# Optimization experiments

Hardware: AMD Instinct MI355X
Metric: run time of the kernel (lower is better)

The kernel has to match this reference:

```python
import jax, jax.numpy as jnp
import numpy as np

N, E, H, NH = 10000, 160000, 128, 8
HD = H // NH
LDIM = 8  # (lmax+1)**2 - 1 with lmax=2
CUTOFF = 5.0


def setup_inputs() -> dict:
    key = jax.random.key(0)
    ks = jax.random.split(key, 20)
    w = lambda k, shape: jax.random.normal(k, shape, jnp.float32) * 0.05
    return dict(
        node_feats=jax.random.normal(ks[0], (N, H), jnp.float32),
        edge_feats=jax.random.normal(ks[1], (E, H), jnp.float32),
        vector_feats=jax.random.normal(ks[2], (N, LDIM, H), jnp.float32),
        distances=jax.random.uniform(ks[3], (E,), jnp.float32) * CUTOFF,
        d_ij=jax.random.normal(ks[4], (E, LDIM), jnp.float32),
        senders=jax.random.randint(ks[5], (E,), 0, N),
        receivers=jax.random.randint(ks[6], (E,), 0, N),
        ln_scale=jnp.ones((H,), jnp.float32),
        ln_bias=jnp.zeros((H,), jnp.float32),
        vln_w=jnp.ones((H,), jnp.float32),
        W_vec=w(ks[7], (H, 3 * H)),
        Wq=w(ks[8], (H, H)), bq=jnp.zeros((H,), jnp.float32),
        Wk=w(ks[9], (H, H)), bk=jnp.zeros((H,), jnp.float32),
        Wv=w(ks[10], (H, H)), bv=jnp.zeros((H,), jnp.float32),
        Wdk=w(ks[11], (H, H)), bdk=jnp.zeros((H,), jnp.float32),
        Wdv=w(ks[12], (H, H)), bdv=jnp.zeros((H,), jnp.float32),
        Ws=w(ks[13], (H, 2 * H)), bs=jnp.zeros((2 * H,), jnp.float32),
        Wo=w(ks[14], (H, 3 * H)), bo=jnp.zeros((3 * H,), jnp.float32),
        Wf=w(ks[15], (H, H)), bf=jnp.zeros((H,), jnp.float32),
        Wsrc=w(ks[16], (H, H)),
        Wtrg=w(ks[17], (H, H)),
    )


def _reject(vec, d):
    # vector rejection of vec [E, L, H] against direction d [E, L]
    proj = (vec * d[:, :, None]).sum(axis=1, keepdims=True)
    return vec - proj * d[:, :, None]


def _forward(node_feats, edge_feats, vector_feats, distances, d_ij, senders, receivers,
             ln_scale, ln_bias, vln_w, W_vec, Wq, bq, Wk, bk, Wv, bv, Wdk, bdk, Wdv, bdv,
             Ws, bs, Wo, bo, Wf, bf, Wsrc, Wtrg):
    silu = jax.nn.silu
    n = node_feats.shape[0]
    # LayerNorm (eps=1e-5) on node feats
    mu = node_feats.mean(-1, keepdims=True)
    xc = node_feats - mu
    var = (xc * xc).mean(-1, keepdims=True)
    x = xc * jax.lax.rsqrt(var + 1e-5) * ln_scale + ln_bias
    # VecLayerNorm with norm_type='none' -> identity norm + learned per-channel scale
    vec = vector_feats * vln_w
    q = (x @ Wq + bq).reshape(-1, NH, HD)
    k = (x @ Wk + bk).reshape(-1, NH, HD)
    v = (x @ Wv + bv).reshape(-1, NH, HD)
    dk = silu(edge_feats @ Wdk + bdk).reshape(-1, NH, HD)
    dv = silu(edge_feats @ Wdv + bdv).reshape(-1, NH, HD)
    vec1, vec2, vec3 = jnp.split(vec @ W_vec, [H, 2 * H], axis=-1)
    vec_dot = (vec1 * vec2).sum(axis=1)  # [N, H]
    # per-edge gathers
    q_i = q[receivers]
    k_j = k[senders]
    v_j = v[senders]
    vec_j = vec[senders]  # [E, LDIM, H]
    # attention-style message with cosine cutoff
    cut = 0.5 * (jnp.cos(distances * (jnp.pi / CUTOFF)) + 1.0) * (distances < CUTOFF)
    attn = silu((q_i * k_j * dk).sum(-1)) * cut[:, None]  # [E, NH]
    vj = ((v_j * dv) * attn[:, :, None]).reshape(-1, H)   # [E, H]
    s1, s2 = jnp.split(silu(vj @ Ws + bs), [H], axis=1)
    vec_msg = vec_j * s1[:, None, :] + s2[:, None, :] * d_ij[:, :, None]
    # scatter reduce to nodes
    node_agg = jax.ops.segment_sum(vj, receivers, num_segments=n)
    vec_agg = jax.ops.segment_sum(vec_msg, receivers, num_segments=n)
    o1, o2, o3 = jnp.split(node_agg @ Wo + bo, [H, 2 * H], axis=1)
    dx = vec_dot * o2 + o3
    dvec = vec3 * o1[:, None, :] + vec_agg
    # edge update (last_layer=False)
    w1 = _reject(vec[receivers] @ Wtrg, d_ij)
    w2 = _reject(vec_j @ Wsrc, -d_ij)
    w_dot = (w1 * w2).sum(axis=1)  # [E, H]
    df_ij = silu(edge_feats @ Wf + bf) * w_dot
    return dx, df_ij, dvec


def reference(node_feats, edge_feats, vector_feats, distances, d_ij, senders, receivers,
              ln_scale, ln_bias, vln_w, W_vec, Wq, bq, Wk, bk, Wv, bv, Wdk, bdk, Wdv, bdv,
              Ws, bs, Wo, bo, Wf, bf, Wsrc, Wtrg):
    return _forward(node_feats, edge_feats, vector_feats, distances, d_ij, senders, receivers,
                    ln_scale, ln_bias, vln_w, W_vec, Wq, bq, Wk, bk, Wv, bv, Wdk, bdk, Wdv, bdv,
                    Ws, bs, Wo, bo, Wf, bf, Wsrc, Wtrg)
```

## Files before the change

### kernel.cpp

```cpp
#include <hip/hip_runtime.h>
#include <math.h>

#define NN 10000
#define NE 160000
#define H  128
#define LD 8

typedef unsigned short ushort_t;
typedef short bf16x8 __attribute__((ext_vector_type(8)));
typedef float f32x4 __attribute__((ext_vector_type(4)));

__device__ __forceinline__ float silu_f(float x){ return x / (1.0f + expf(-x)); }
__device__ __forceinline__ float4 f4z(){ return make_float4(0.f,0.f,0.f,0.f); }

__device__ __forceinline__ void fma4(float4& acc, float s, const float4 w){
    acc.x = fmaf(s, w.x, acc.x);
    acc.y = fmaf(s, w.y, acc.y);
    acc.z = fmaf(s, w.z, acc.z);
    acc.w = fmaf(s, w.w, acc.w);
}

__device__ __forceinline__ float4 silu4(float4 a, float4 b){
    return make_float4(silu_f(a.x+b.x), silu_f(a.y+b.y), silu_f(a.z+b.z), silu_f(a.w+b.w));
}

__device__ __forceinline__ ushort_t f2bf(float f){
    union { float f; unsigned int u; } x; x.f = f;
    unsigned int r = x.u + 0x7FFFu + ((x.u >> 16) & 1u);
    return (ushort_t)(r >> 16);
}
__device__ __forceinline__ unsigned int pack2bf(float a, float b){
    return (unsigned int)f2bf(a) | ((unsigned int)f2bf(b) << 16);
}
__device__ __forceinline__ float bf2f_hi(unsigned int u){
    union { unsigned int u; float f; } x; x.u = u & 0xffff0000u; return x.f;
}
__device__ __forceinline__ float bf2f_lo(unsigned int u){
    union { unsigned int u; float f; } x; x.u = u << 16; return x.f;
}

__global__ void k_prepw(const float* __restrict__ Wq, const float* __restrict__ Wk,
                        const float* __restrict__ Wv, const float* __restrict__ W_vec,
                        const float* __restrict__ Wtrg, const float* __restrict__ Wsrc,
                        const float* __restrict__ Wdk, const float* __restrict__ Wdv,
                        const float* __restrict__ Ws,
                        ushort_t* __restrict__ wqkvT, ushort_t* __restrict__ wvecT,
                        ushort_t* __restrict__ wdkT, ushort_t* __restrict__ wdvT,
                        ushort_t* __restrict__ wsT){
    int i = blockIdx.x * 256 + threadIdx.x;
    int n = i >> 7, kk = i & 127;
    if (n < 384){
        float v;
        if (n < 128)      v = Wq[kk*128 + n];
        else if (n < 256) v = Wk[kk*128 + (n-128)];
        else              v = Wv[kk*128 + (n-256)];
        wqkvT[n*128 + kk] = f2bf(v);
    } else if (n < 1024){
        int m = n - 384;
        float v;
        if (m < 384)      v = W_vec[kk*384 + m];
        else if (m < 512) v = Wtrg[kk*128 + (m-384)];
        else              v = Wsrc[kk*128 + (m-512)];
        wvecT[m*128 + kk] = f2bf(v);
    } else if (n < 1152){
        int m = n - 1024;
        wdkT[m*128 + kk] = f2bf(Wdk[kk*128 + m]);
    } else if (n < 1280){
        int m = n - 1152;
        wdvT[m*128 + kk] = f2bf(Wdv[kk*128 + m]);
    } else if (n < 1536){
        int m = n - 1280;
        wsT[m*128 + kk] = f2bf(Ws[kk*256 + m]);
    }
}

__global__ void k_ef2bf(const float* __restrict__ ef, ushort_t* __restrict__ ef_bf){
    size_t i = (size_t)blockIdx.x * 256 + threadIdx.x;
    const float4* s = (const float4*)ef;
    float4 a = s[2*i], b = s[2*i+1];
    uint4 u;
    u.x = pack2bf(a.x, a.y); u.y = pack2bf(a.z, a.w);
    u.z = pack2bf(b.x, b.y); u.w = pack2bf(b.z, b.w);
    ((uint4*)ef_bf)[i] = u;
}

__global__ void k_hist(const int* __restrict__ rcv, int* __restrict__ cnt){
    int e = blockIdx.x * 256 + threadIdx.x;
    if (e < NE) atomicAdd(&cnt[rcv[e]], 1);
}

__global__ __launch_bounds__(256) void k_scan(const int* __restrict__ cnt, int* __restrict__ offs){
    __shared__ int part[256];
    const int t = threadIdx.x;
    const int CH = 40;
    int loc[CH];
    int base = t * CH;
    int lsum = 0;
    if (base < NN){
        #pragma unroll
        for (int i = 0; i < CH; i++){ loc[i] = cnt[base + i]; lsum += loc[i]; }
    }
    part[t] = lsum;
    __syncthreads();
    for (int off = 1; off < 256; off <<= 1){
        int v = (t >= off) ? part[t - off] : 0;
        __syncthreads();
        part[t] += v;
        __syncthreads();
    }
    int ex = part[t] - lsum;
    if (base < NN){
        int run = ex;
        #pragma unroll
        for (int i = 0; i < CH; i++){ offs[base + i] = run; run += loc[i]; }
    }
    if (t == 255) offs[NN] = part[255];
}

__global__ void k_scatter(const int* __restrict__ rcv, const int* __restrict__ offs,
                          int* __restrict__ cnt2, int* __restrict__ eidx){
    int e = blockIdx.x * 256 + threadIdx.x;
    if (e < NE){
        int r = rcv[e];
        int p = atomicAdd(&cnt2[r], 1);
        eidx[offs[r] + p] = e;
    }
}

__global__ __launch_bounds__(128) void node_ln(
    const float* __restrict__ nf, const float* __restrict__ vf,
    const float* __restrict__ ln_s, const float* __restrict__ ln_b,
    const float* __restrict__ vlnw,
    ushort_t* __restrict__ x_bf, ushort_t* __restrict__ vec_bf)
{
    const int n = blockIdx.x, h = threadIdx.x;
    __shared__ float red[4];
    float xv = nf[(size_t)n*H + h];
    float s1 = xv, s2 = xv*xv;
    #pragma unroll
    for (int o = 32; o >= 1; o >>= 1){
        s1 += __shfl_xor(s1, o, 64);
        s2 += __shfl_xor(s2, o, 64);
    }
    const int wid = h >> 6;
    if ((h & 63) == 0){ red[wid] = s1; red[2+wid] = s2; }
    __syncthreads();
    float mean = (red[0] + red[1]) * (1.0f/H);
    float var  = (red[2] + red[3]) * (1.0f/H) - mean*mean;
    float x = (xv - mean) * rsqrtf(var + 1e-5f) * ln_s[h] + ln_b[h];
    x_bf[(size_t)n*H + h] = f2bf(x);
    float w = vlnw[h];
    #pragma unroll
    for (int l = 0; l < LD; l++){
        size_t i = ((size_t)n*LD + l)*H + h;
        vec_bf[i] = f2bf(vf[i] * w);
    }
}

__global__ __launch_bounds__(256) void node_qkv(
    const ushort_t* __restrict__ x_bf, const ushort_t* __restrict__ wqkvT,
    const float* __restrict__ bq, const float* __restrict__ bk, const float* __restrict__ bv,
    float* __restrict__ q, float* __restrict__ k, float* __restrict__ v)
{
    const int tid  = threadIdx.x;
    const int lane = tid & 63;
    const int m0   = (tid >> 6) * 16;
    const int e0   = blockIdx.x * 64;

    const int mrow = lane & 15;
    const int kblk = lane >> 4;

    f32x4 acc[24];
    #pragma unroll
    for (int nt = 0; nt < 24; nt++) acc[nt] = (f32x4)(0.f);

    int arow = e0 + m0 + mrow; if (arow >= NN) arow = NN-1;
    const ushort_t* Arow = x_bf + (size_t)arow*H + kblk*8;
    const ushort_t* wb   = wqkvT + (size_t)mrow*H + kblk*8;

    #pragma unroll
    for (int ks = 0; ks < 4; ks++){
        bf16x8 a = *(const bf16x8*)(Arow + ks*32);
        #pragma unroll
        for (int nt = 0; nt < 24; nt++){
            bf16x8 b8 = *(const bf16x8*)(wb + (size_t)nt*16*H + ks*32);
            acc[nt] = __builtin_amdgcn_mfma_f32_16x16x32_bf16(a, b8, acc[nt], 0, 0, 0);
        }
    }
    float* outs[3] = {q, k, v};
    const float* bias[3] = {bq, bk, bv};
    #pragma unroll
    for (int g = 0; g < 3; g++){
        #pragma unroll
        for (int t = 0; t < 8; t++){
            int col = t*16 + mrow;
            float bb = bias[g][col];
            #pragma unroll
            for (int r = 0; r < 4; r++){
                int row = e0 + m0 + kblk*4 + r;
                if (row < NN) outs[g][(size_t)row*H + col] = acc[g*8+t][r] + bb;
            }
        }
    }
}

__global__ __launch_bounds__(256) void node_vec(
    const ushort_t* __restrict__ vec_bf, const ushort_t* __restrict__ wvecT,
    float* __restrict__ vdot, ushort_t* __restrict__ vec3,
    ushort_t* __restrict__ Vt, ushort_t* __restrict__ Vs)
{
    __shared__ ushort_t st_s[64][136];

    const int tid  = threadIdx.x;
    const int lane = tid & 63;
    const int wv   = tid >> 6;
    const int m0   = wv * 16;
    const size_t r0 = (size_t)blockIdx.x * 64;

    const int mrow = lane & 15;
    const int kblk = lane >> 4;

    f32x4 acc[40];
    #pragma unroll
    for (int nt = 0; nt < 40; nt++) acc[nt] = (f32x4)(0.f);

    const ushort_t* Arow = vec_bf + (r0 + m0 + mrow)*H + kblk*8;
    const ushort_t* wb   = wvecT + (size_t)mrow*H + kblk*8;

    #pragma unroll
    for (int ks = 0; ks < 4; ks++){
        bf16x8 a = *(const bf16x8*)(Arow + ks*32);
        #pragma unroll
        for (int nt = 0; nt < 40; nt++){
            bf16x8 b8 = *(const bf16x8*)(wb + (size_t)nt*16*H + ks*32);
            acc[nt] = __builtin_amdgcn_mfma_f32_16x16x32_bf16(a, b8, acc[nt], 0, 0, 0);
        }
    }

    #pragma unroll
    for (int t = 0; t < 8; t++){
        float p = acc[t][0]*acc[t+8][0] + acc[t][1]*acc[t+8][1]
                + acc[t][2]*acc[t+8][2] + acc[t][3]*acc[t+8][3];
        p += __shfl_xor(p, 16, 64);
        if ((kblk & 1) == 0){
            int node = (int)(r0 >> 3) + wv*2 + (kblk >> 1);
            vdot[(size_t)node*H + t*16 + mrow] = p;
        }
    }

    ushort_t* outs[3] = {vec3, Vt, Vs};
    #pragma unroll
    for (int g = 0; g < 3; g++){
        __syncthreads();
        #pragma unroll
        for (int t = 0; t < 8; t++){
            int coln = t*16 + mrow;
            int lr = m0 + kblk*4;
            st_s[lr+0][coln] = f2bf(acc[16+g*8+t][0]);
            st_s[lr+1][coln] = f2bf(acc[16+g*8+t][1]);
            st_s[lr+2][coln] = f2bf(acc[16+g*8+t][2]);
            st_s[lr+3][coln] = f2bf(acc[16+g*8+t][3]);
        }
        __syncthreads();
        const int rr = tid >> 2, qq = tid & 3;
        uint4* dst = (uint4*)&outs[g][(r0 + rr)*H + qq*32];
        const uint4* src = (const uint4*)&st_s[rr][qq*32];
        dst[0] = src[0]; dst[1] = src[1]; dst[2] = src[2]; dst[3] = src[3];
    }
}

__global__ __launch_bounds__(256) void edge_attn(
    const ushort_t* __restrict__ ef_bf,
    const ushort_t* __restrict__ wdkT, const float* __restrict__ bdk,
    const ushort_t* __restrict__ wdvT, const float* __restrict__ bdv,
    const int* __restrict__ snd, const int* __restrict__ rcv,
    const float* __restrict__ dist,
    const float* __restrict__ q, const float* __restrict__ k, const float* __restrict__ v,
    ushort_t* __restrict__ vj)
{
    __shared__ ushort_t dk_s[64][136];
    __shared__ ushort_t dv_s[64][136];

    const int tid  = threadIdx.x;
    const int lane = tid & 63;
    const int m0   = (tid >> 6) * 16;
    const size_t e0 = (size_t)blockIdx.x * 64;

    const int mrow = lane & 15;
    const int kblk = lane >> 4;

    f32x4 accK[8], accV[8];
    #pragma unroll
    for (int nt = 0; nt < 8; nt++){ accK[nt] = (f32x4)(0.f); accV[nt] = (f32x4)(0.f); }

    const ushort_t* Arow = ef_bf + (e0 + m0 + mrow)*H + kblk*8;
    const ushort_t* wkb  = wdkT + (size_t)mrow*H + kblk*8;
    const ushort_t* wvb  = wdvT + (size_t)mrow*H + kblk*8;

    #pragma unroll
    for (int ks = 0; ks < 4; ks++){
        bf16x8 a = *(const bf16x8*)(Arow + ks*32);
        #pragma unroll
        for (int nt = 0; nt < 8; nt++){
            bf16x8 bk8 = *(const bf16x8*)(wkb + (size_t)nt*16*H + ks*32);
            accK[nt] = __builtin_amdgcn_mfma_f32_16x16x32_bf16(a, bk8, accK[nt], 0, 0, 0);
            bf16x8 bv8 = *(const bf16x8*)(wvb + (size_t)nt*16*H + ks*32);
            accV[nt] = __builtin_amdgcn_mfma_f32_16x16x32_bf16(a, bv8, accV[nt], 0, 0, 0);
        }
    }

    const int lrow = m0 + 4*kblk;
    #pragma unroll
    for (int nt = 0; nt < 8; nt++){
        int coln = nt*16 + mrow;
        float bkn = bdk[coln], bvn = bdv[coln];
        #pragma unroll
        for (int r = 0; r < 4; r++){
            dk_s[lrow + r][coln] = f2bf(silu_f(accK[nt][r] + bkn));
            dv_s[lrow + r][coln] = f2bf(silu_f(accV[nt][r] + bvn));
        }
    }
    __syncthreads();

    const int r  = tid >> 2, cq = tid & 3;
    const size_t e = e0 + r;
    const int s  = snd[e], rr = rcv[e];
    const float d = dist[e];
    const float cut = (d < 5.0f) ? 0.5f*(cosf(d*0.6283185307179586f) + 1.0f) : 0.0f;
    const float* qrow = q + (size_t)rr*H + cq*32;
    const float* krow = k + (size_t)s*H + cq*32;
    const float* vrow = v + (size_t)s*H + cq*32;
    ushort_t* vjrow = vj + e*H + cq*32;

    #pragma unroll
    for (int hh = 0; hh < 2; hh++){
        const int c0 = hh*16;
        float p = 0.f;
        #pragma unroll
        for (int j = 0; j < 4; j++){
            float4 q4 = *(const float4*)(qrow + c0 + 4*j);
            float4 k4 = *(const float4*)(krow + c0 + 4*j);
            uint2 du = *(const uint2*)&dk_s[r][cq*32 + c0 + 4*j];
            p += q4.x*k4.x*bf2f_lo(du.x) + q4.y*k4.y*bf2f_hi(du.x)
               + q4.z*k4.z*bf2f_lo(du.y) + q4.w*k4.w*bf2f_hi(du.y);
        }
        float attn = silu_f(p) * cut;
        #pragma unroll
        for (int j = 0; j < 4; j++){
            float4 v4 = *(const float4*)(vrow + c0 + 4*j);
            uint2 du = *(const uint2*)&dv_s[r][cq*32 + c0 + 4*j];
            uint2 u;
            u.x = pack2bf(v4.x*bf2f_lo(du.x)*attn, v4.y*bf2f_hi(du.x)*attn);
            u.y = pack2bf(v4.z*bf2f_lo(du.y)*attn, v4.w*bf2f_hi(du.y)*attn);
            *(uint2*)(vjrow + c0 + 4*j) = u;
        }
    }
}

__global__ __launch_bounds__(256) void edge_s(
    const ushort_t* __restrict__ vj, const ushort_t* __restrict__ wsT,
    const float* __restrict__ bs, ushort_t* __restrict__ s12)
{
    __shared__ ushort_t s_s[64][264];

    const int tid  = threadIdx.x;
    const int lane = tid & 63;
    const int m0   = (tid >> 6) * 16;
    const size_t e0 = (size_t)blockIdx.x * 64;

    const int mrow = lane & 15;
    const int kblk = lane >> 4;

    f32x4 acc[16];
    #pragma unroll
    for (int nt = 0; nt < 16; nt++) acc[nt] = (f32x4)(0.f);

    const ushort_t* Arow = vj + (e0 + m0 + mrow)*H + kblk*8;
    const ushort_t* wb   = wsT + (size_t)mrow*H + kblk*8;

    #pragma unroll
    for (int ks = 0; ks < 4; ks++){
        bf16x8 a = *(const bf16x8*)(Arow + ks*32);
        #pragma unroll
        for (int nt = 0; nt < 16; nt++){
            bf16x8 b8 = *(const bf16x8*)(wb + (size_t)nt*16*H + ks*32);
            acc[nt] = __builtin_amdgcn_mfma_f32_16x16x32_bf16(a, b8, acc[nt], 0, 0, 0);
        }
    }

    const int lrow = m0 + 4*kblk;
    #pragma unroll
    for (int nt = 0; nt < 16; nt++){
        int coln = nt*16 + mrow;
        float bb = bs[coln];
        #pragma unroll
        for (int r = 0; r < 4; r++)
            s_s[lrow + r][coln] = f2bf(silu_f(acc[nt][r] + bb));
    }
    __syncthreads();

    const int r = tid >> 2, cq = tid & 3;
    const uint4* srcp = (const uint4*)&s_s[r][cq*64];
    uint4* dstp = (uint4*)&s12[(e0 + r)*256 + cq*64];
    #pragma unroll
    for (int j = 0; j < 8; j++) dstp[j] = srcp[j];
}

__global__ __launch_bounds__(256) void edge_df(
    const float* __restrict__ ef, const float* __restrict__ Wf, const float* __restrict__ bf_,
    const int* __restrict__ eidx,
    const int* __restrict__ snd, const int* __restrict__ rcv,
    const float* __restrict__ dij,
    const ushort_t* __restrict__ Vt, const ushort_t* __restrict__ Vs,
    float* __restrict__ df)
{
    __shared__ float wf_s[H][32];
    __shared__ float e_s[32][H+4];
    __shared__ int   eidx_s[32];
    __shared__ int   snd_s[32];
    __shared__ int   rcv_s[32];
    __shared__ float dij_s[32][LD];

    const int tid = threadIdx.x;
    const int by  = blockIdx.y;
    const int p0  = blockIdx.x * 32;

    if (tid < 32) eidx_s[tid] = eidx[p0 + tid];
    __syncthreads();
    if (tid < 32){ int e = eidx_s[tid]; snd_s[tid] = snd[e]; rcv_s[tid] = rcv[e]; }
    for (int i = tid; i < 32*LD; i += 256){
        int row = i >> 3, l = i & 7;
        dij_s[row][l] = dij[(size_t)eidx_s[row]*LD + l];
    }
    for (int i = tid; i < H*8; i += 256){
        int row = i >> 3, c4 = i & 7;
        *(float4*)&wf_s[row][c4*4] = *(const float4*)&Wf[row*H + by*32 + c4*4];
    }
    for (int i = tid; i < 32*32; i += 256){
        int row = i >> 5, c4 = i & 31;
        *(float4*)&e_s[row][c4*4] = *(const float4*)&ef[(size_t)eidx_s[row]*H + c4*4];
    }
    __syncthreads();

    const int g = tid & 7, r0 = tid >> 3;
    float4 af = f4z();
    for (int kk = 0; kk < H; kk++){
        float4 w4 = *(float4*)&wf_s[kk][g*4];
        fma4(af, e_s[r0][kk], w4);
    }
    float4 bf4 = *(const float4*)&bf_[by*32 + g*4];
    float4 f4v = silu4(af, bf4);

    const int e = eidx_s[r0];
    const int s = snd_s[r0], rr = rcv_s[r0];
    const ushort_t* Ar = Vt + (size_t)rr*LD*H + by*32 + g*4;
    const ushort_t* Br = Vs + (size_t)s*LD*H + by*32 + g*4;

    float4 AB = f4z(), aa = f4z(), bb = f4z();
    float dd = 0.f;
    #pragma unroll
    for (int l = 0; l < LD; l++){
        float dl = dij_s[r0][l];
        dd = fmaf(dl, dl, dd);
        uint2 ua = *(const uint2*)&Ar[(size_t)l*H];
        uint2 ub = *(const uint2*)&Br[(size_t)l*H];
        float Ax = bf2f_lo(ua.x), Ay = bf2f_hi(ua.x), Az = bf2f_lo(ua.y), Aw = bf2f_hi(ua.y);
        float Bx = bf2f_lo(ub.x), By = bf2f_hi(ub.x), Bz = bf2f_lo(ub.y), Bw = bf2f_hi(ub.y);
        AB.x = fmaf(Ax, Bx, AB.x); AB.y = fmaf(Ay, By, AB.y);
        AB.z = fmaf(Az, Bz, AB.z); AB.w = fmaf(Aw, Bw, AB.w);
        aa.x = fmaf(Ax, dl, aa.x); aa.y = fmaf(Ay, dl, aa.y);
        aa.z = fmaf(Az, dl, aa.z); aa.w = fmaf(Aw, dl, aa.w);
        bb.x = fmaf(Bx, dl, bb.x); bb.y = fmaf(By, dl, bb.y);
        bb.z = fmaf(Bz, dl, bb.z); bb.w = fmaf(Bw, dl, bb.w);
    }
    float c = 2.0f - dd;
    float4 o = make_float4(f4v.x*(AB.x - aa.x*bb.x*c),
                           f4v.y*(AB.y - aa.y*bb.y*c),
                           f4v.z*(AB.z - aa.z*bb.z*c),
                           f4v.w*(AB.w - aa.w*bb.w*c));
    *(float4*)&df[(size_t)e*H + by*32 + g*4] = o;
}

__global__ __launch_bounds__(256) void node_gather(
    const int* __restrict__ offs, const int* __restrict__ eidx, const int* __restrict__ snd,
    const ushort_t* __restrict__ vj, const ushort_t* __restrict__ s12,
    const float* __restrict__ dij, const ushort_t* __restrict__ vec,
    const float* __restrict__ Wo, const float* __restrict__ bo,
    const float* __restrict__ vdot, const ushort_t* __restrict__ vec3,
    float* __restrict__ dx, float* __restrict__ dvec)
{
    const int n = blockIdx.x;
    const int tid = threadIdx.x;
    const int h = tid & 127;
    const int par = tid >> 7;
    const int beg = offs[n], end = offs[n+1];
    float na = 0.f;
    float av[LD];
    #pragma unroll
    for (int l = 0; l < LD; l++) av[l] = 0.f;

    for (int i = beg + par; i < end; i += 2){
        int e = eidx[i];
        int s = snd[e];
        float vjv = bf2f_lo((unsigned int)vj[(size_t)e*H + h]);
        float s1 = bf2f_lo((unsigned int)s12[(size_t)e*256 + h]);
        float s2 = bf2f_lo((unsigned int)s12[(size_t)e*256 + 128 + h]);
        na += vjv;
        float4 d0 = *(const float4*)&dij[(size_t)e*LD];
        float4 d1 = *(const float4*)&dij[(size_t)e*LD + 4];
        const ushort_t* vr = &vec[(size_t)s*LD*H + h];
        av[0] = fmaf(bf2f_lo((unsigned int)vr[0*H]), s1, fmaf(d0.x, s2, av[0]));
        av[1] = fmaf(bf2f_lo((unsigned int)vr[1*H]), s1, fmaf(d0.y, s2, av[1]));
        av[2] = fmaf(bf2f_lo((unsigned int)vr[2*H]), s1, fmaf(d0.z, s2, av[2]));
        av[3] = fmaf(bf2f_lo((unsigned int)vr[3*H]), s1, fmaf(d0.w, s2, av[3]));
        av[4] = fmaf(bf2f_lo((unsigned int)vr[4*H]), s1, fmaf(d1.x, s2, av[4]));
        av[5] = fmaf(bf2f_lo((unsigned int)vr[5*H]), s1, fmaf(d1.y, s2, av[5]));
        av[6] = fmaf(bf2f_lo((unsigned int)vr[6*H]), s1, fmaf(d1.z, s2, av[6]));
        av[7] = fmaf(bf2f_lo((unsigned int)vr[7*H]), s1, fmaf(d1.w, s2, av[7]));
    }

    __shared__ float red_s[LD+1][128];
    if (par == 0){
        #pragma unroll
        for (int l = 0; l < LD; l++) red_s[l][h] = av[l];
        red_s[LD][h] = na;
    }
    __syncthreads();
    if (par == 1){
        #pragma unroll
        for (int l = 0; l < LD; l++) red_s[l][h] += av[l];
        red_s[LD][h] += na;
    }
    __syncthreads();

    if (par == 0){
        float o1 = bo[h], o2 = bo[H + h], o3 = bo[2*H + h];
        for (int kk = 0; kk < H; kk++){
            float a = red_s[LD][kk];
            o1 = fmaf(a, Wo[kk*(3*H) + h], o1);
            o2 = fmaf(a, Wo[kk*(3*H) + H + h], o2);
            o3 = fmaf(a, Wo[kk*(3*H) + 2*H + h], o3);
        }
        dx[(size_t)n*H + h] = fmaf(vdot[(size_t)n*H + h], o2, o3);
        #pragma unroll
        for (int l = 0; l < LD; l++){
            size_t i2 = ((size_t)n*LD + l)*H + h;
            dvec[i2] = fmaf(bf2f_lo((unsigned int)vec3[i2]), o1, red_s[l][h]);
        }
    }
}

extern "C" void kernel_launch(void* const* d_in, const int* in_sizes, int n_in,
                              void* d_out, int out_size, void* d_ws, size_t ws_size,
                              hipStream_t stream) {
    const float* nf    = (const float*)d_in[0];
    const float* ef    = (const float*)d_in[1];
    const float* vf    = (const float*)d_in[2];
    const float* dist  = (const float*)d_in[3];
    const float* dij   = (const float*)d_in[4];
    const int*   snd   = (const int*)d_in[5];
    const int*   rcv   = (const int*)d_in[6];
    const float* ln_s  = (const float*)d_in[7];
    const float* ln_b  = (const float*)d_in[8];
    const float* vlnw  = (const float*)d_in[9];
    const float* W_vec = (const float*)d_in[10];
    const float* Wq    = (const float*)d_in[11];
    const float* bq    = (const float*)d_in[12];
    const float* Wk    = (const float*)d_in[13];
    const float* bk    = (const float*)d_in[14];
    const float* Wv    = (const float*)d_in[15];
    const float* bv    = (const float*)d_in[16];
    const float* Wdk   = (const float*)d_in[17];
    const float* bdk   = (const float*)d_in[18];
    const float* Wdv   = (const float*)d_in[19];
    const float* bdv   = (const float*)d_in[20];
    const float* Ws    = (const float*)d_in[21];
    const float* bs    = (const float*)d_in[22];
    const float* Wo    = (const float*)d_in[23];
    const float* bo    = (const float*)d_in[24];
    const float* Wf    = (const float*)d_in[25];
    const float* bf_   = (const float*)d_in[26];
    const float* Wsrc  = (const float*)d_in[27];
    const float* Wtrg  = (const float*)d_in[28];

    float* out  = (float*)d_out;
    float* dx   = out;
    float* df   = out + (size_t)NN*H;
    float* dvec = df + (size_t)NE*H;

    float* w = (float*)d_ws;
    size_t off = 0;
    float* q    = w + off; off += (size_t)NN*H;
    float* k    = w + off; off += (size_t)NN*H;
    float* v    = w + off; off += (size_t)NN*H;
    float* vdot = w + off; off += (size_t)NN*H;
    ushort_t* x_bf   = (ushort_t*)(w + off); off += (size_t)NN*H/2;
    ushort_t* vec_bf = (ushort_t*)(w + off); off += (size_t)NN*LD*H/2;
    ushort_t* vec3   = (ushort_t*)(w + off); off += (size_t)NN*LD*H/2;
    ushort_t* Vt     = (ushort_t*)(w + off); off += (size_t)NN*LD*H/2;
    ushort_t* Vs     = (ushort_t*)(w + off); off += (size_t)NN*LD*H/2;
    ushort_t* vj     = (ushort_t*)(w + off); off += (size_t)NE*H/2;
    ushort_t* s12    = (ushort_t*)(w + off); off += (size_t)NE*256/2;
    ushort_t* ef_bf  = s12;
    ushort_t* wqkvT = (ushort_t*)(w + off); off += 384*128/2;
    ushort_t* wvecT = (ushort_t*)(w + off); off += 640*128/2;
    ushort_t* wdkT  = (ushort_t*)(w + off); off += 128*128/2;
    ushort_t* wdvT  = (ushort_t*)(w + off); off += 128*128/2;
    ushort_t* wsT   = (ushort_t*)(w + off); off += 256*128/2;
    int* cnt  = (int*)(w + off); off += NN;
    int* cnt2 = (int*)(w + off); off += NN;
    int* offs = (int*)(w + off); off += NN + 1;
    int* eidx = (int*)(w + off); off += NE;

    hipMemsetAsync(cnt,  0, NN*sizeof(int), stream);
    hipMemsetAsync(cnt2, 0, NN*sizeof(int), stream);

    k_prepw<<<768, 256, 0, stream>>>(Wq, Wk, Wv, W_vec, Wtrg, Wsrc, Wdk, Wdv, Ws,
                                     wqkvT, wvecT, wdkT, wdvT, wsT);
    k_ef2bf<<<NE*H/8/256, 256, 0, stream>>>(ef, ef_bf);

    k_hist<<<(NE+255)/256, 256, 0, stream>>>(rcv, cnt);
    k_scan<<<1, 256, 0, stream>>>(cnt, offs);
    k_scatter<<<(NE+255)/256, 256, 0, stream>>>(rcv, offs, cnt2, eidx);

    node_ln<<<NN, 128, 0, stream>>>(nf, vf, ln_s, ln_b, vlnw, x_bf, vec_bf);

    node_qkv<<<(NN+63)/64, 256, 0, stream>>>(x_bf, wqkvT, bq, bk, bv, q, k, v);

    node_vec<<<NN*LD/64, 256, 0, stream>>>(vec_bf, wvecT, vdot, vec3, Vt, Vs);

    edge_attn<<<NE/64, 256, 0, stream>>>(ef_bf, wdkT, bdk, wdvT, bdv, snd, rcv, dist,
                                         q, k, v, vj);

    edge_df<<<dim3(NE/32, 4), 256, 0, stream>>>(ef, Wf, bf_, eidx, snd, rcv, dij, Vt, Vs, df);

    edge_s<<<NE/64, 256, 0, stream>>>(vj, wsT, bs, s12);

    node_gather<<<NN, 256, 0, stream>>>(offs, eidx, snd, vj, s12, dij, vec_bf,
                                        Wo, bo, vdot, vec3, dx, dvec);
}
```

Measured before the change: 831.7 us.

## Store k/v in bf16, widen edge_df column tile, and split node_gather four ways

Three separate changes. The k and v projections are stored as bf16 so the per-edge sender gathers in edge_attn read half the bytes. edge_df now handles 64 columns per block with two row passes, halving how often edge_feats is reloaded and the matmul redone across the y grid. node_gather runs 512 threads, splits edges four ways, and spreads the Wo projection over three thread groups. Together these add bf16 rounding on k and v, more shared memory, and an extra barrier in node_gather.

```diff
diff --git a/kernel.cpp b/kernel.cpp
--- a/kernel.cpp
+++ b/kernel.cpp
@@ -160,7 +160,7 @@
 __global__ __launch_bounds__(256) void node_qkv(
     const ushort_t* __restrict__ x_bf, const ushort_t* __restrict__ wqkvT,
     const float* __restrict__ bq, const float* __restrict__ bk, const float* __restrict__ bv,
-    float* __restrict__ q, float* __restrict__ k, float* __restrict__ v)
+    float* __restrict__ q, ushort_t* __restrict__ k_bf, ushort_t* __restrict__ v_bf)
 {
     const int tid  = threadIdx.x;
     const int lane = tid & 63;
@@ -187,19 +187,34 @@
             acc[nt] = __builtin_amdgcn_mfma_f32_16x16x32_bf16(a, b8, acc[nt], 0, 0, 0);
         }
     }
-    float* outs[3] = {q, k, v};
-    const float* bias[3] = {bq, bk, bv};
-    #pragma unroll
-    for (int g = 0; g < 3; g++){
-        #pragma unroll
-        for (int t = 0; t < 8; t++){
-            int col = t*16 + mrow;
-            float bb = bias[g][col];
-            #pragma unroll
-            for (int r = 0; r < 4; r++){
-                int row = e0 + m0 + kblk*4 + r;
-                if (row < NN) outs[g][(size_t)row*H + col] = acc[g*8+t][r] + bb;
-            }
+    #pragma unroll
+    for (int t = 0; t < 8; t++){
+        int col = t*16 + mrow;
+        float bb = bq[col];
+        #pragma unroll
+        for (int r = 0; r < 4; r++){
+            int row = e0 + m0 + kblk*4 + r;
+            if (row < NN) q[(size_t)row*H + col] = acc[t][r] + bb;
+        }
+    }
+    #pragma unroll
+    for (int t = 0; t < 8; t++){
+        int col = t*16 + mrow;
+        float bb = bk[col];
+        #pragma unroll
+        for (int r = 0; r < 4; r++){
+            int row = e0 + m0 + kblk*4 + r;
+            if (row < NN) k_bf[(size_t)row*H + col] = f2bf(acc[8+t][r] + bb);
+        }
+    }
+    #pragma unroll
+    for (int t = 0; t < 8; t++){
+        int col = t*16 + mrow;
+        float bb = bv[col];
+        #pragma unroll
+        for (int r = 0; r < 4; r++){
+            int row = e0 + m0 + kblk*4 + r;
+            if (row < NN) v_bf[(size_t)row*H + col] = f2bf(acc[16+t][r] + bb);
         }
     }
 }
@@ -275,7 +290,8 @@
     const ushort_t* __restrict__ wdvT, const float* __restrict__ bdv,
     const int* __restrict__ snd, const int* __restrict__ rcv,
     const float* __restrict__ dist,
-    const float* __restrict__ q, const float* __restrict__ k, const float* __restrict__ v,
+    const float* __restrict__ q, const ushort_t* __restrict__ k_bf,
+    const ushort_t* __restrict__ v_bf,
     ushort_t* __restrict__ vj)
 {
     __shared__ ushort_t dk_s[64][136];
@@ -327,9 +343,9 @@
     const int s  = snd[e], rr = rcv[e];
     const float d = dist[e];
     const float cut = (d < 5.0f) ? 0.5f*(cosf(d*0.6283185307179586f) + 1.0f) : 0.0f;
-    const float* qrow = q + (size_t)rr*H + cq*32;
-    const float* krow = k + (size_t)s*H + cq*32;
-    const float* vrow = v + (size_t)s*H + cq*32;
+    const float*    qrow = q    + (size_t)rr*H + cq*32;
+    const ushort_t* krow = k_bf + (size_t)s*H + cq*32;
+    const ushort_t* vrow = v_bf + (size_t)s*H + cq*32;
     ushort_t* vjrow = vj + e*H + cq*32;
 
     #pragma unroll
@@ -339,19 +355,21 @@
         #pragma unroll
         for (int j = 0; j < 4; j++){
             float4 q4 = *(const float4*)(qrow + c0 + 4*j);
-            float4 k4 = *(const float4*)(krow + c0 + 4*j);
+            uint2 ku = *(const uint2*)(krow + c0 + 4*j);
             uint2 du = *(const uint2*)&dk_s[r][cq*32 + c0 + 4*j];
-            p += q4.x*k4.x*bf2f_lo(du.x) + q4.y*k4.y*bf2f_hi(du.x)
-               + q4.z*k4.z*bf2f_lo(du.y) + q4.w*k4.w*bf2f_hi(du.y);
+            p += q4.x*bf2f_lo(ku.x)*bf2f_lo(du.x) + q4.y*bf2f_hi(ku.x)*bf2f_hi(du.x)
+               + q4.z*bf2f_lo(ku.y)*bf2f_lo(du.y) + q4.w*bf2f_hi(ku.y)*bf2f_hi(du.y);
         }
         float attn = silu_f(p) * cut;
         #pragma unroll
         for (int j = 0; j < 4; j++){
-            float4 v4 = *(const float4*)(vrow + c0 + 4*j);
+            uint2 vu = *(const uint2*)(vrow + c0 + 4*j);
             uint2 du = *(const uint2*)&dv_s[r][cq*32 + c0 + 4*j];
             uint2 u;
-            u.x = pack2bf(v4.x*bf2f_lo(du.x)*attn, v4.y*bf2f_hi(du.x)*attn);
-            u.y = pack2bf(v4.z*bf2f_lo(du.y)*attn, v4.w*bf2f_hi(du.y)*attn);
+            u.x = pack2bf(bf2f_lo(vu.x)*bf2f_lo(du.x)*attn,
+                          bf2f_hi(vu.x)*bf2f_hi(du.x)*attn);
+            u.y = pack2bf(bf2f_lo(vu.y)*bf2f_lo(du.y)*attn,
+                          bf2f_hi(vu.y)*bf2f_hi(du.y)*attn);
             *(uint2*)(vjrow + c0 + 4*j) = u;
         }
     }
@@ -414,7 +432,7 @@
     const ushort_t* __restrict__ Vt, const ushort_t* __restrict__ Vs,
     float* __restrict__ df)
 {
-    __shared__ float wf_s[H][32];
+    __shared__ float wf_s[H][64];
     __shared__ float e_s[32][H+4];
     __shared__ int   eidx_s[32];
     __shared__ int   snd_s[32];
@@ -432,9 +450,9 @@
         int row = i >> 3, l = i & 7;
         dij_s[row][l] = dij[(size_t)eidx_s[row]*LD + l];
     }
-    for (int i = tid; i < H*8; i += 256){
-        int row = i >> 3, c4 = i & 7;
-        *(float4*)&wf_s[row][c4*4] = *(const float4*)&Wf[row*H + by*32 + c4*4];
+    for (int i = tid; i < H*16; i += 256){
+        int row = i >> 4, c4 = i & 15;
+        *(float4*)&wf_s[row][c4*4] = *(const float4*)&Wf[row*H + by*64 + c4*4];
     }
     for (int i = tid; i < 32*32; i += 256){
         int row = i >> 5, c4 = i & 31;
@@ -442,46 +460,50 @@
     }
     __syncthreads();
 
-    const int g = tid & 7, r0 = tid >> 3;
-    float4 af = f4z();
-    for (int kk = 0; kk < H; kk++){
-        float4 w4 = *(float4*)&wf_s[kk][g*4];
-        fma4(af, e_s[r0][kk], w4);
-    }
-    float4 bf4 = *(const float4*)&bf_[by*32 + g*4];
-    float4 f4v = silu4(af, bf4);
-
-    const int e = eidx_s[r0];
-    const int s = snd_s[r0], rr = rcv_s[r0];
-    const ushort_t* Ar = Vt + (size_t)rr*LD*H + by*32 + g*4;
-    const ushort_t* Br = Vs + (size_t)s*LD*H + by*32 + g*4;
-
-    float4 AB = f4z(), aa = f4z(), bb = f4z();
-    float dd = 0.f;
-    #pragma unroll
-    for (int l = 0; l < LD; l++){
-        float dl = dij_s[r0][l];
-        dd = fmaf(dl, dl, dd);
-        uint2 ua = *(const uint2*)&Ar[(size_t)l*H];
-        uint2 ub = *(const uint2*)&Br[(size_t)l*H];
-        float Ax = bf2f_lo(ua.x), Ay = bf2f_hi(ua.x), Az = bf2f_lo(ua.y), Aw = bf2f_hi(ua.y);
-        float Bx = bf2f_lo(ub.x), By = bf2f_hi(ub.x), Bz = bf2f_lo(ub.y), Bw = bf2f_hi(ub.y);
-        AB.x = fmaf(Ax, Bx, AB.x); AB.y = fmaf(Ay, By, AB.y);
-        AB.z = fmaf(Az, Bz, AB.z); AB.w = fmaf(Aw, Bw, AB.w);
-        aa.x = fmaf(Ax, dl, aa.x); aa.y = fmaf(Ay, dl, aa.y);
-        aa.z = fmaf(Az, dl, aa.z); aa.w = fmaf(Aw, dl, aa.w);
-        bb.x = fmaf(Bx, dl, bb.x); bb.y = fmaf(By, dl, bb.y);
-        bb.z = fmaf(Bz, dl, bb.z); bb.w = fmaf(Bw, dl, bb.w);
-    }
-    float c = 2.0f - dd;
-    float4 o = make_float4(f4v.x*(AB.x - aa.x*bb.x*c),
-                           f4v.y*(AB.y - aa.y*bb.y*c),
-                           f4v.z*(AB.z - aa.z*bb.z*c),
-                           f4v.w*(AB.w - aa.w*bb.w*c));
-    *(float4*)&df[(size_t)e*H + by*32 + g*4] = o;
-}
-
-__global__ __launch_bounds__(256) void node_gather(
+    const int g = tid & 15, r0 = tid >> 4;
+    #pragma unroll
+    for (int pass = 0; pass < 2; pass++){
+        const int rr = r0 + pass*16;
+        float4 af = f4z();
+        for (int kk = 0; kk < H; kk++){
+            float4 w4 = *(float4*)&wf_s[kk][g*4];
+            fma4(af, e_s[rr][kk], w4);
+        }
+        float4 bf4 = *(const float4*)&bf_[by*64 + g*4];
+        float4 f4v = silu4(af, bf4);
+
+        const int e = eidx_s[rr];
+        const int s = snd_s[rr], rn = rcv_s[rr];
+        const ushort_t* Ar = Vt + (size_t)rn*LD*H + by*64 + g*4;
+        const ushort_t* Br = Vs + (size_t)s*LD*H + by*64 + g*4;
+
+        float4 AB = f4z(), aa = f4z(), bb = f4z();
+        float dd = 0.f;
+        #pragma unroll
+        for (int l = 0; l < LD; l++){
+            float dl = dij_s[rr][l];
+            dd = fmaf(dl, dl, dd);
+            uint2 ua = *(const uint2*)&Ar[(size_t)l*H];
+            uint2 ub = *(const uint2*)&Br[(size_t)l*H];
+            float Ax = bf2f_lo(ua.x), Ay = bf2f_hi(ua.x), Az = bf2f_lo(ua.y), Aw = bf2f_hi(ua.y);
+            float Bx = bf2f_lo(ub.x), By = bf2f_hi(ub.x), Bz = bf2f_lo(ub.y), Bw = bf2f_hi(ub.y);
+            AB.x = fmaf(Ax, Bx, AB.x); AB.y = fmaf(Ay, By, AB.y);
+            AB.z = fmaf(Az, Bz, AB.z); AB.w = fmaf(Aw, Bw, AB.w);
+            aa.x = fmaf(Ax, dl, aa.x); aa.y = fmaf(Ay, dl, aa.y);
+            aa.z = fmaf(Az, dl, aa.z); aa.w = fmaf(Aw, dl, aa.w);
+            bb.x = fmaf(Bx, dl, bb.x); bb.y = fmaf(By, dl, bb.y);
+            bb.z = fmaf(Bz, dl, bb.z); bb.w = fmaf(Bw, dl, bb.w);
+        }
+        float c = 2.0f - dd;
+        float4 o = make_float4(f4v.x*(AB.x - aa.x*bb.x*c),
+                               f4v.y*(AB.y - aa.y*bb.y*c),
+                               f4v.z*(AB.z - aa.z*bb.z*c),
+                               f4v.w*(AB.w - aa.w*bb.w*c));
+        *(float4*)&df[(size_t)e*H + by*64 + g*4] = o;
+    }
+}
+
+__global__ __launch_bounds__(512) void node_gather(
     const int* __restrict__ offs, const int* __restrict__ eidx, const int* __restrict__ snd,
     const ushort_t* __restrict__ vj, const ushort_t* __restrict__ s12,
     const float* __restrict__ dij, const ushort_t* __restrict__ vec,
@@ -499,7 +521,7 @@
     #pragma unroll
     for (int l = 0; l < LD; l++) av[l] = 0.f;
 
-    for (int i = beg + par; i < end; i += 2){
+    for (int i = beg + par; i < end; i += 4){
         int e = eidx[i];
         int s = snd[e];
         float vjv = bf2f_lo((unsigned int)vj[(size_t)e*H + h]);
@@ -519,33 +541,35 @@
         av[7] = fmaf(bf2f_lo((unsigned int)vr[7*H]), s1, fmaf(d1.w, s2, av[7]));
     }
 
-    __shared__ float red_s[LD+1][128];
+    __shared__ float pl[4][LD+1][128];
+    __shared__ float o_s[3][128];
+    #pragma unroll
+    for (int l = 0; l < LD; l++) pl[par][l][h] = av[l];
+    pl[par][LD][h] = na;
+    __syncthreads();
+
     if (par == 0){
         #pragma unroll
-        for (int l = 0; l < LD; l++) red_s[l][h] = av[l];
-        red_s[LD][h] = na;
-    }
-    __syncthreads();
-    if (par == 1){
-        #pragma unroll
-        for (int l = 0; l < LD; l++) red_s[l][h] += av[l];
-        red_s[LD][h] += na;
+        for (int l = 0; l <= LD; l++)
+            pl[0][l][h] = (pl[0][l][h] + pl[1][l][h]) + (pl[2][l][h] + pl[3][l][h]);
+    }
+    __syncthreads();
+
+    if (par > 0){
+        const int g = par - 1;
+        float o = bo[g*H + h];
+        for (int kk = 0; kk < H; kk++)
+            o = fmaf(pl[0][LD][kk], Wo[kk*(3*H) + g*H + h], o);
+        o_s[g][h] = o;
     }
     __syncthreads();
 
     if (par == 0){
-        float o1 = bo[h], o2 = bo[H + h], o3 = bo[2*H + h];
-        for (int kk = 0; kk < H; kk++){
-            float a = red_s[LD][kk];
-            o1 = fmaf(a, Wo[kk*(3*H) + h], o1);
-            o2 = fmaf(a, Wo[kk*(3*H) + H + h], o2);
-            o3 = fmaf(a, Wo[kk*(3*H) + 2*H + h], o3);
-        }
-        dx[(size_t)n*H + h] = fmaf(vdot[(size_t)n*H + h], o2, o3);
+        dx[(size_t)n*H + h] = fmaf(vdot[(size_t)n*H + h], o_s[1][h], o_s[2][h]);
         #pragma unroll
         for (int l = 0; l < LD; l++){
             size_t i2 = ((size_t)n*LD + l)*H + h;
-            dvec[i2] = fmaf(bf2f_lo((unsigned int)vec3[i2]), o1, red_s[l][h]);
+            dvec[i2] = fmaf(bf2f_lo((unsigned int)vec3[i2]), o_s[0][h], pl[0][l][h]);
         }
     }
 }
@@ -591,9 +615,9 @@
     float* w = (float*)d_ws;
     size_t off = 0;
     float* q    = w + off; off += (size_t)NN*H;
-    float* k    = w + off; off += (size_t)NN*H;
-    float* v    = w + off; off += (size_t)NN*H;
     float* vdot = w + off; off += (size_t)NN*H;
+    ushort_t* k_bf   = (ushort_t*)(w + off); off += (size_t)NN*H/2;
+    ushort_t* v_bf   = (ushort_t*)(w + off); off += (size_t)NN*H/2;
     ushort_t* x_bf   = (ushort_t*)(w + off); off += (size_t)NN*H/2;
     ushort_t* vec_bf = (ushort_t*)(w + off); off += (size_t)NN*LD*H/2;
     ushort_t* vec3   = (ushort_t*)(w + off); off += (size_t)NN*LD*H/2;
@@ -625,17 +649,18 @@
 
     node_ln<<<NN, 128, 0, stream>>>(nf, vf, ln_s, ln_b, vlnw, x_bf, vec_bf);
 
-    node_qkv<<<(NN+63)/64, 256, 0, stream>>>(x_bf, wqkvT, bq, bk, bv, q, k, v);
+    node_qkv<<<(NN+63)/64, 256, 0, stream>>>(x_bf, wqkvT, bq, bk, bv, q, k_bf, v_bf);
 
     node_vec<<<NN*LD/64, 256, 0, stream>>>(vec_bf, wvecT, vdot, vec3, Vt, Vs);
 
     edge_attn<<<NE/64, 256, 0, stream>>>(ef_bf, wdkT, bdk, wdvT, bdv, snd, rcv, dist,
-                                         q, k, v, vj);
-
-    edge_df<<<dim3(NE/32, 4), 256, 0, stream>>>(ef, Wf, bf_, eidx, snd, rcv, dij, Vt, Vs, df);
+                                         q, k_bf, v_bf, vj);
+
+    edge_df<<<dim3(NE/32, 2), 256, 0, stream>>>(ef, Wf, bf_, eidx, snd, rcv, dij,
+                                                Vt, Vs, df);
 
     edge_s<<<NE/64, 256, 0, stream>>>(vj, wsT, bs, s12);
 
-    node_gather<<<NN, 256, 0, stream>>>(offs, eidx, snd, vj, s12, dij, vec_bf,
+    node_gather<<<NN, 512, 0, stream>>>(offs, eidx, snd, vj, s12, dij, vec_bf,
                                         Wo, bo, vdot, vec3, dx, dvec);
 }
```

After: 809.2 us, median of 2. 1.03x faster.
